# Kernel optimization log

Measured on AMD Instinct MI355X. Metric: run time of the kernel, lower is better.

Reference implementation:

```python
import jax, jax.numpy as jnp
import numpy as np

N, IN_DIM, OUT_DIM, HEADS = 50000, 128, 32, 8
E = 800000
F = OUT_DIM * HEADS  # 256 fused output features
SEM_HID = 128        # SemanticAttention hidden size (HAN default)


def setup_inputs() -> dict:
    key = jax.random.key(0)
    ks = jax.random.split(key, 16)
    inp = {
        "h": jax.random.normal(ks[0], (N, IN_DIM), jnp.float32),
        "src_a": jax.random.randint(ks[1], (E,), 0, N, jnp.int32),
        "dst_a": jax.random.randint(ks[2], (E,), 0, N, jnp.int32),
        "src_b": jax.random.randint(ks[3], (E,), 0, N, jnp.int32),
        "dst_b": jax.random.randint(ks[4], (E,), 0, N, jnp.int32),
    }
    s = 1.0 / np.sqrt(IN_DIM)
    # per-metapath GATConv params
    inp["W_a"] = jax.random.normal(ks[5], (IN_DIM, F), jnp.float32) * s
    inp["al_a"] = jax.random.normal(ks[6], (HEADS, OUT_DIM), jnp.float32) * 0.1
    inp["ar_a"] = jax.random.normal(ks[7], (HEADS, OUT_DIM), jnp.float32) * 0.1
    inp["bias_a"] = jnp.zeros((F,), jnp.float32)
    inp["W_b"] = jax.random.normal(ks[8], (IN_DIM, F), jnp.float32) * s
    inp["al_b"] = jax.random.normal(ks[9], (HEADS, OUT_DIM), jnp.float32) * 0.1
    inp["ar_b"] = jax.random.normal(ks[10], (HEADS, OUT_DIM), jnp.float32) * 0.1
    inp["bias_b"] = jnp.zeros((F,), jnp.float32)
    # semantic attention params
    inp["Wsem"] = jax.random.normal(ks[11], (F, SEM_HID), jnp.float32) / np.sqrt(F)
    inp["bsem"] = jnp.zeros((SEM_HID,), jnp.float32)
    inp["wsem"] = jax.random.normal(ks[12], (SEM_HID,), jnp.float32) / np.sqrt(SEM_HID)
    return inp


def gat_conv(h, src, dst, W, al, ar, bias):
    # h: [N, in_dim] -> feat: [N, H, D]
    feat = (h @ W).reshape(N, HEADS, OUT_DIM)
    el = (feat * al).sum(-1)  # [N, H]
    er = (feat * ar).sum(-1)  # [N, H]
    e = jax.nn.leaky_relu(el[src] + er[dst], 0.2)  # [E, H]
    # edge softmax over incoming edges of each dst node (numerically stable)
    m = jax.ops.segment_max(e, dst, num_segments=N)        # -inf for empty
    ex = jnp.exp(e - m[dst])                               # [E, H]
    denom = jax.ops.segment_sum(ex, dst, num_segments=N)   # [N, H]
    msg = feat[src] * ex[:, :, None]                       # [E, H, D]
    out = jax.ops.segment_sum(msg, dst, num_segments=N)    # [N, H, D]
    out = out / jnp.where(denom > 0, denom, 1.0)[:, :, None]
    return jax.nn.elu(out.reshape(N, F) + bias)


def reference(h, src_a, dst_a, src_b, dst_b,
              W_a, al_a, ar_a, bias_a,
              W_b, al_b, ar_b, bias_b,
              Wsem, bsem, wsem):
    z_a = gat_conv(h, src_a, dst_a, W_a, al_a, ar_a, bias_a)
    z_b = gat_conv(h, src_b, dst_b, W_b, al_b, ar_b, bias_b)
    z = jnp.stack([z_a, z_b], axis=1)                 # [N, M, F]
    q = jnp.tanh(z @ Wsem + bsem) @ wsem              # [N, M]
    beta = jax.nn.softmax(q.mean(axis=0))             # [M]
    return (z * beta[None, :, None]).sum(axis=1)      # [N, F]
```

## Files before the change

kernel.cpp:

```cpp
#include <hip/hip_runtime.h>
#include <stdint.h>

#define NN 50000
#define EE 800000
#define IN_DIM 128
#define OUT_DIM 32
#define HEADS 8
#define FF 256
#define SH 128
#define NPAD 50048
#define FEXT 272
#define NBLK_SCAN 196

typedef short s16x8 __attribute__((ext_vector_type(8)));
typedef float f32x4 __attribute__((ext_vector_type(4)));

__device__ __forceinline__ float b2f(unsigned short u) {
    union { unsigned int i; float f; } v; v.i = ((unsigned int)u) << 16; return v.f;
}
__device__ __forceinline__ unsigned short f2b(float f) {
    union { float f; unsigned int i; } v; v.f = f;
    unsigned int i = v.i;
    unsigned int r = (i + 0x7FFFu + ((i >> 16) & 1u)) >> 16;
    return (unsigned short)r;
}

#define PREP_WSEMT   128
#define PREP_H2B     6256
#define PREP_G       (PREP_WSEMT + PREP_H2B + FEXT + FEXT)

__device__ __forceinline__ void buildBT_one(
    const float* __restrict__ W, const float* __restrict__ al,
    const float* __restrict__ ar, unsigned short* __restrict__ BT,
    int fp, int k)
{
    float v;
    if (fp < FF) {
        v = W[(size_t)k * FF + fp];
    } else if (fp < FF + 8) {
        int hh = fp - FF;
        float s = 0.f;
        #pragma unroll
        for (int d = 0; d < 32; ++d) s += W[(size_t)k * FF + hh * 32 + d] * al[hh * 32 + d];
        v = s;
    } else {
        int hh = fp - FF - 8;
        float s = 0.f;
        #pragma unroll
        for (int d = 0; d < 32; ++d) s += W[(size_t)k * FF + hh * 32 + d] * ar[hh * 32 + d];
        v = s;
    }
    BT[(size_t)fp * IN_DIM + k] = f2b(v);
}

__global__ __launch_bounds__(256) void prep_kernel(
    const float* __restrict__ Wsem, unsigned short* __restrict__ WsemT,
    const float* __restrict__ h, unsigned short* __restrict__ hb,
    const float* __restrict__ W_a, const float* __restrict__ al_a,
    const float* __restrict__ ar_a, unsigned short* __restrict__ BT_a,
    const float* __restrict__ W_b, const float* __restrict__ al_b,
    const float* __restrict__ ar_b, unsigned short* __restrict__ BT_b)
{
    int b = blockIdx.x, t = threadIdx.x;
    if (b < PREP_WSEMT) {
        WsemT[b * FF + t] = f2b(Wsem[(size_t)t * SH + b]);
    } else if (b < PREP_WSEMT + PREP_H2B) {
        int i = ((b - PREP_WSEMT) * 256 + t) * 4;
        int row = i >> 7;
        ushort4 r;
        if (row < NN) {
            float4 v = *(const float4*)(h + i);
            r.x = f2b(v.x); r.y = f2b(v.y); r.z = f2b(v.z); r.w = f2b(v.w);
        } else {
            r.x = r.y = r.z = r.w = 0;
        }
        *(ushort4*)(hb + i) = r;
    } else if (b < PREP_WSEMT + PREP_H2B + FEXT) {
        if (t < IN_DIM) buildBT_one(W_a, al_a, ar_a, BT_a, b - PREP_WSEMT - PREP_H2B, t);
    } else {
        if (t < IN_DIM) buildBT_one(W_b, al_b, ar_b, BT_b, b - PREP_WSEMT - PREP_H2B - FEXT, t);
    }
}

__global__ void rank_both(const int* __restrict__ dst_a, const int* __restrict__ dst_b,
                          int* __restrict__ counts_a, int* __restrict__ counts_b,
                          unsigned short* __restrict__ rank_a, unsigned short* __restrict__ rank_b)
{
    int idx = blockIdx.x * blockDim.x + threadIdx.x;
    if (idx < EE) {
        rank_a[idx] = (unsigned short)atomicAdd(&counts_a[dst_a[idx]], 1);
    } else {
        int e = idx - EE;
        rank_b[e] = (unsigned short)atomicAdd(&counts_b[dst_b[e]], 1);
    }
}

__global__ __launch_bounds__(256) void scan1_both(
    const int* __restrict__ counts_a, const int* __restrict__ counts_b,
    int* __restrict__ offs_a, int* __restrict__ offs_b,
    int* __restrict__ bsums_a, int* __restrict__ bsums_b)
{
    __shared__ int sm[256];
    int bb = blockIdx.x;
    const int* counts = (bb < NBLK_SCAN) ? counts_a : counts_b;
    int* offs  = (bb < NBLK_SCAN) ? offs_a  : offs_b;
    int* bsums = (bb < NBLK_SCAN) ? bsums_a : bsums_b;
    int blk = (bb < NBLK_SCAN) ? bb : bb - NBLK_SCAN;
    int t = threadIdx.x, i = blk * 256 + t;
    int v = (i < NN) ? counts[i] : 0;
    sm[t] = v; __syncthreads();
    for (int d = 1; d < 256; d <<= 1) {
        int x = (t >= d) ? sm[t - d] : 0;
        __syncthreads();
        sm[t] += x;
        __syncthreads();
    }
    if (i < NN) offs[i] = sm[t] - v;
    if (t == 255) bsums[blk] = sm[255];
}

__global__ __launch_bounds__(256) void scan2_both(
    int* __restrict__ bsums_a, int* __restrict__ bsums_b,
    int* __restrict__ offs_a, int* __restrict__ offs_b)
{
    __shared__ int sm[256];
    int* bsums = blockIdx.x ? bsums_b : bsums_a;
    int* offs  = blockIdx.x ? offs_b  : offs_a;
    int t = threadIdx.x;
    int v = (t < NBLK_SCAN) ? bsums[t] : 0;
    sm[t] = v; __syncthreads();
    for (int d = 1; d < 256; d <<= 1) {
        int x = (t >= d) ? sm[t - d] : 0;
        __syncthreads();
        sm[t] += x;
        __syncthreads();
    }
    if (t < NBLK_SCAN) bsums[t] = sm[t] - v;
    if (t == 0) offs[NN] = EE;
}

__global__ __launch_bounds__(256) void scan3_both(
    int* __restrict__ offs_a, int* __restrict__ offs_b,
    const int* __restrict__ bsums_a, const int* __restrict__ bsums_b)
{
    int bb = blockIdx.x;
    int* offs = (bb < NBLK_SCAN) ? offs_a : offs_b;
    const int* bsums = (bb < NBLK_SCAN) ? bsums_a : bsums_b;
    int blk = (bb < NBLK_SCAN) ? bb : bb - NBLK_SCAN;
    int t = threadIdx.x, i = blk * 256 + t;
    if (i < NN) offs[i] += bsums[blk];
}

__global__ void fill_both(const int* __restrict__ src_a, const int* __restrict__ dst_a,
                          const int* __restrict__ src_b, const int* __restrict__ dst_b,
                          const int* __restrict__ offs_a, const int* __restrict__ offs_b,
                          const unsigned short* __restrict__ rank_a,
                          const unsigned short* __restrict__ rank_b,
                          unsigned short* __restrict__ perm_a,
                          unsigned short* __restrict__ perm_b)
{
    int idx = blockIdx.x * blockDim.x + threadIdx.x;
    if (idx < EE) {
        int d = dst_a[idx];
        int slot = offs_a[d] + rank_a[idx];
        perm_a[slot] = (unsigned short)src_a[idx];
    } else {
        int e = idx - EE;
        int d = dst_b[e];
        int slot = offs_b[d] + rank_b[e];
        perm_b[slot] = (unsigned short)src_b[e];
    }
}

__global__ __launch_bounds__(256) void gemm_feat_mfma(
    const unsigned short* __restrict__ hb,
    const unsigned short* __restrict__ BT,
    unsigned short* __restrict__ feat,
    float* __restrict__ el, float* __restrict__ er)
{
    int wave = threadIdx.x >> 6, lane = threadIdx.x & 63;
    int quad = lane >> 4, l16 = lane & 15;
    int nbase = blockIdx.x * 64 + wave * 16;
    int n = nbase + l16;
    const unsigned short* arow = hb + (size_t)n * IN_DIM + quad * 8;
    s16x8 nfr[4];
    #pragma unroll
    for (int kt = 0; kt < 4; ++kt)
        nfr[kt] = *(const s16x8*)(arow + kt * 32);
    bool live = (n < NN);
    #pragma unroll 1
    for (int ft = 0; ft < 17; ++ft) {
        const unsigned short* brow = BT + (size_t)(ft * 16 + l16) * IN_DIM + quad * 8;
        f32x4 c = {0.f, 0.f, 0.f, 0.f};
        #pragma unroll
        for (int kt = 0; kt < 4; ++kt) {
            s16x8 ffr = *(const s16x8*)(brow + kt * 32);
            c = __builtin_amdgcn_mfma_f32_16x16x32_bf16(ffr, nfr[kt], c, 0, 0, 0);
        }
        if (ft < 16) {
            if (live) {
                ushort4 r;
                r.x = f2b(c[0]); r.y = f2b(c[1]); r.z = f2b(c[2]); r.w = f2b(c[3]);
                *(ushort4*)(feat + (size_t)n * FF + ft * 16 + quad * 4) = r;
            }
        } else {
            if (live) {
                #pragma unroll
                for (int r = 0; r < 4; ++r) {
                    int jp = quad * 4 + r;
                    if (jp < 8) el[n * HEADS + jp] = c[r];
                    else        er[n * HEADS + (jp - 8)] = c[r];
                }
            }
        }
    }
}

__global__ __launch_bounds__(256) void pull_kernel(
    const int* __restrict__ offs, const unsigned short* __restrict__ src_perm,
    const float* __restrict__ el, const float* __restrict__ er,
    const unsigned short* __restrict__ feat,
    const float* __restrict__ bias, unsigned short* __restrict__ zb)
{
    int wave = threadIdx.x >> 6;
    int lane = threadIdx.x & 63;
    int n = blockIdx.x * 4 + wave;
    if (n >= NN) return;
    int head = lane >> 3;
    int f0 = lane * 4;
    int j0 = offs[n], j1 = offs[n + 1];
    float ern = er[n * HEADS + head];
    float den = 0.f;
    float a0 = 0.f, a1 = 0.f, a2 = 0.f, a3 = 0.f;

#define EDGE_STEP(S) {                                              \
        float x = el[(S) * HEADS + head] + ern;                     \
        x = fmaxf(x, 0.2f * x);                                     \
        float ex = __expf(x);                                       \
        den += ex;                                                  \
        ushort4 fv = *(const ushort4*)(feat + (size_t)(S) * FF + f0);\
        a0 += b2f(fv.x) * ex;                                       \
        a1 += b2f(fv.y) * ex;                                       \
        a2 += b2f(fv.z) * ex;                                       \
        a3 += b2f(fv.w) * ex; }

    int j = j0;
    for (; j + 8 <= j1; j += 8) {
        int s0 = src_perm[j + 0];
        int s1 = src_perm[j + 1];
        int s2 = src_perm[j + 2];
        int s3 = src_perm[j + 3];
        int s4 = src_perm[j + 4];
        int s5 = src_perm[j + 5];
        int s6 = src_perm[j + 6];
        int s7 = src_perm[j + 7];
        EDGE_STEP(s0); EDGE_STEP(s1); EDGE_STEP(s2); EDGE_STEP(s3);
        EDGE_STEP(s4); EDGE_STEP(s5); EDGE_STEP(s6); EDGE_STEP(s7);
    }
    if (j + 4 <= j1) {
        int s0 = src_perm[j + 0];
        int s1 = src_perm[j + 1];
        int s2 = src_perm[j + 2];
        int s3 = src_perm[j + 3];
        EDGE_STEP(s0); EDGE_STEP(s1); EDGE_STEP(s2); EDGE_STEP(s3);
        j += 4;
    }
    for (; j < j1; ++j) {
        int s = src_perm[j];
        EDGE_STEP(s);
    }
#undef EDGE_STEP

    if (den <= 0.f) den = 1.f;
    float inv = 1.f / den;
    float4 bv = *(const float4*)(bias + f0);
    float o0 = a0 * inv + bv.x;
    float o1 = a1 * inv + bv.y;
    float o2 = a2 * inv + bv.z;
    float o3 = a3 * inv + bv.w;
    ushort4 rb;
    rb.x = f2b((o0 > 0.f) ? o0 : (__expf(o0) - 1.f));
    rb.y = f2b((o1 > 0.f) ? o1 : (__expf(o1) - 1.f));
    rb.z = f2b((o2 > 0.f) ? o2 : (__expf(o2) - 1.f));
    rb.w = f2b((o3 > 0.f) ? o3 : (__expf(o3) - 1.f));
    *(ushort4*)(zb + (size_t)n * FF + f0) = rb;
}

__global__ __launch_bounds__(256) void sem_mfma_kernel(
    const unsigned short* __restrict__ zb,
    const unsigned short* __restrict__ WsemT,
    const float* __restrict__ bsem, const float* __restrict__ wsem,
    float* __restrict__ qsum, int idx)
{
    int wave = threadIdx.x >> 6, lane = threadIdx.x & 63;
    int quad = lane >> 4, l16 = lane & 15;
    int nbase = blockIdx.x * 64 + wave * 16;
    const unsigned short* arow = zb + (size_t)(nbase + l16) * FF + quad * 8;
    s16x8 afr[8];
    #pragma unroll
    for (int kt = 0; kt < 8; ++kt)
        afr[kt] = *(const s16x8*)(arow + kt * 32);
    float qacc = 0.f;
    for (int jt = 0; jt < 8; ++jt) {
        int jj = jt * 16 + l16;
        const unsigned short* brow = WsemT + (size_t)jj * FF + quad * 8;
        f32x4 c = {0.f, 0.f, 0.f, 0.f};
        #pragma unroll
        for (int kt = 0; kt < 8; ++kt) {
            s16x8 bfr = *(const s16x8*)(brow + kt * 32);
            c = __builtin_amdgcn_mfma_f32_16x16x32_bf16(afr[kt], bfr, c, 0, 0, 0);
        }
        float bj = bsem[jj], wj = wsem[jj];
        #pragma unroll
        for (int r = 0; r < 4; ++r) {
            int n = nbase + quad * 4 + r;
            float tv = tanhf(c[r] + bj) * wj;
            qacc += (n < NN) ? tv : 0.f;
        }
    }
    #pragma unroll
    for (int o = 1; o < 64; o <<= 1) qacc += __shfl_xor(qacc, o, 64);
    __shared__ float wsum[4];
    if (lane == 0) wsum[wave] = qacc;
    __syncthreads();
    if (threadIdx.x == 0)
        atomicAdd(&qsum[idx], wsum[0] + wsum[1] + wsum[2] + wsum[3]);
}

__global__ void combine_kernel(const unsigned short* __restrict__ za,
                               const unsigned short* __restrict__ zbm,
                               float* __restrict__ out,
                               const float* __restrict__ qsum)
{
    size_t i = (size_t)blockIdx.x * blockDim.x + threadIdx.x;
    size_t base = i * 4;
    if (base >= (size_t)NN * FF) return;
    float qa = qsum[0] * (1.f / NN), qb = qsum[1] * (1.f / NN);
    float mx = fmaxf(qa, qb);
    float ea = __expf(qa - mx), eb = __expf(qb - mx);
    float inv = 1.f / (ea + eb);
    float b0 = ea * inv, b1 = eb * inv;
    ushort4 va = *(const ushort4*)(za + base);
    ushort4 vb = *(const ushort4*)(zbm + base);
    float4 r;
    r.x = b0 * b2f(va.x) + b1 * b2f(vb.x);
    r.y = b0 * b2f(va.y) + b1 * b2f(vb.y);
    r.z = b0 * b2f(va.z) + b1 * b2f(vb.z);
    r.w = b0 * b2f(va.w) + b1 * b2f(vb.w);
    *(float4*)(out + base) = r;
}

extern "C" void kernel_launch(void* const* d_in, const int* in_sizes, int n_in,
                              void* d_out, int out_size, void* d_ws, size_t ws_size,
                              hipStream_t stream)
{
    const float* h      = (const float*)d_in[0];
    const int* src_a    = (const int*)d_in[1];
    const int* dst_a    = (const int*)d_in[2];
    const int* src_b    = (const int*)d_in[3];
    const int* dst_b    = (const int*)d_in[4];
    const float* W_a    = (const float*)d_in[5];
    const float* al_a   = (const float*)d_in[6];
    const float* ar_a   = (const float*)d_in[7];
    const float* bias_a = (const float*)d_in[8];
    const float* W_b    = (const float*)d_in[9];
    const float* al_b   = (const float*)d_in[10];
    const float* ar_b   = (const float*)d_in[11];
    const float* bias_b = (const float*)d_in[12];
    const float* Wsem   = (const float*)d_in[13];
    const float* bsem   = (const float*)d_in[14];
    const float* wsem   = (const float*)d_in[15];
    float* out = (float*)d_out;

    char* ws = (char*)d_ws;
    size_t o = 0;
    auto alloc = [&](size_t bytes) -> char* {
        char* p = ws + o;
        o += (bytes + 255) & ~(size_t)255;
        return p;
    };
    unsigned short* hb    = (unsigned short*)alloc((size_t)NPAD * IN_DIM * 2);
    unsigned short* BT_a  = (unsigned short*)alloc((size_t)FEXT * IN_DIM * 2);
    unsigned short* BT_b  = (unsigned short*)alloc((size_t)FEXT * IN_DIM * 2);
    unsigned short* feat  = (unsigned short*)alloc((size_t)NN * FF * 2);
    unsigned short* zb_a  = (unsigned short*)alloc((size_t)NPAD * FF * 2);
    unsigned short* zb_b  = (unsigned short*)alloc((size_t)NPAD * FF * 2);
    unsigned short* WsemT = (unsigned short*)alloc((size_t)SH * FF * 2);
    float* el_a    = (float*)alloc((size_t)NN * HEADS * 4);
    float* er_a    = (float*)alloc((size_t)NN * HEADS * 4);
    float* el_b    = (float*)alloc((size_t)NN * HEADS * 4);
    float* er_b    = (float*)alloc((size_t)NN * HEADS * 4);
    int* offs_a    = (int*)alloc((size_t)(NN + 1) * 4);
    int* offs_b    = (int*)alloc((size_t)(NN + 1) * 4);
    int* bsums_a   = (int*)alloc(256 * 4);
    int* bsums_b   = (int*)alloc(256 * 4);
    unsigned short* rank_a = (unsigned short*)alloc((size_t)EE * 2);
    unsigned short* rank_b = (unsigned short*)alloc((size_t)EE * 2);
    unsigned short* perm_a = (unsigned short*)alloc((size_t)EE * 2);
    unsigned short* perm_b = (unsigned short*)alloc((size_t)EE * 2);
    char* zspan0   = ws + o;
    int* counts_a  = (int*)alloc((size_t)NN * 4);
    int* counts_b  = (int*)alloc((size_t)NN * 4);
    float* qsum    = (float*)alloc(8);
    size_t zspan   = (size_t)((ws + o) - zspan0);

    prep_kernel<<<PREP_G, 256, 0, stream>>>(Wsem, WsemT, h, hb,
                                            W_a, al_a, ar_a, BT_a,
                                            W_b, al_b, ar_b, BT_b);
    hipMemsetAsync(zspan0, 0, zspan, stream);
    rank_both<<<2 * (EE / 256), 256, 0, stream>>>(dst_a, dst_b, counts_a, counts_b, rank_a, rank_b);
    scan1_both<<<2 * NBLK_SCAN, 256, 0, stream>>>(counts_a, counts_b, offs_a, offs_b, bsums_a, bsums_b);
    scan2_both<<<2, 256, 0, stream>>>(bsums_a, bsums_b, offs_a, offs_b);
    scan3_both<<<2 * NBLK_SCAN, 256, 0, stream>>>(offs_a, offs_b, bsums_a, bsums_b);
    fill_both<<<2 * (EE / 256), 256, 0, stream>>>(src_a, dst_a, src_b, dst_b,
                                                  offs_a, offs_b, rank_a, rank_b, perm_a, perm_b);
    for (int mp = 0; mp < 2; ++mp) {
        const unsigned short* BT = mp ? BT_b : BT_a;
        const float* bias = mp ? bias_b : bias_a;
        float* el = mp ? el_b : el_a;
        float* er = mp ? er_b : er_a;
        const int* offs = mp ? offs_b : offs_a;
        const unsigned short* perm = mp ? perm_b : perm_a;
        unsigned short* zb = mp ? zb_b : zb_a;

        gemm_feat_mfma<<<NPAD / 64, 256, 0, stream>>>(hb, BT, feat, el, er);
        pull_kernel<<<(NN + 3) / 4, 256, 0, stream>>>(offs, perm, el, er, feat, bias, zb);
        sem_mfma_kernel<<<NPAD / 64, 256, 0, stream>>>(zb, WsemT, bsem, wsem, qsum, mp);
    }
    combine_kernel<<<(int)(((size_t)NN * FF / 4 + 255) / 256), 256, 0, stream>>>(zb_a, zb_b, out, qsum);
}
```

Before: 500.3 us.

## Merge independent stages of both metapaths into shared multi-role kernel launches

Regroups independent work into fewer, larger launches. Edge ranking is co-launched with the weight prep, and the CSR fill with both metapaths' feature GEMMs. The two pull passes and the two semantic-attention passes each become a single launch, which cuts launch count and tail idle between small kernels. The separate h-to-bf16 prepass is removed: the GEMM now reads fp32 h and converts in registers, at the cost of reading h twice and converting it per metapath. It also keeps a second feat buffer so both metapaths can be in flight at once, using more workspace memory.

```diff
diff --git a/kernel.cpp b/kernel.cpp
--- a/kernel.cpp
+++ b/kernel.cpp
@@ -12,6 +12,20 @@
 #define FEXT 272
 #define NBLK_SCAN 196
 
+#define RANK_G   6250
+#define A_WSEMT0 6250
+#define A_BTA0   (A_WSEMT0 + 128)
+#define A_BTB0   (A_BTA0 + FEXT)
+#define A_G      (A_BTB0 + FEXT)
+
+#define B_FILL   6250
+#define GEMM_BLKS 782
+#define B_G      (B_FILL + 2 * GEMM_BLKS)
+
+#define PULL_G   12500
+#define C_G      (2 * PULL_G)
+#define D_G      (2 * GEMM_BLKS)
+
 typedef short s16x8 __attribute__((ext_vector_type(8)));
 typedef float f32x4 __attribute__((ext_vector_type(4)));
 
@@ -24,10 +38,6 @@
     unsigned int r = (i + 0x7FFFu + ((i >> 16) & 1u)) >> 16;
     return (unsigned short)r;
 }
-
-#define PREP_WSEMT   128
-#define PREP_H2B     6256
-#define PREP_G       (PREP_WSEMT + PREP_H2B + FEXT + FEXT)
 
 __device__ __forceinline__ void buildBT_one(
     const float* __restrict__ W, const float* __restrict__ al,
@@ -53,45 +63,32 @@
     BT[(size_t)fp * IN_DIM + k] = f2b(v);
 }
 
-__global__ __launch_bounds__(256) void prep_kernel(
+__global__ __launch_bounds__(256) void megaA(
+    const int* __restrict__ dst_a, const int* __restrict__ dst_b,
+    int* __restrict__ counts_a, int* __restrict__ counts_b,
+    unsigned short* __restrict__ rank_a, unsigned short* __restrict__ rank_b,
     const float* __restrict__ Wsem, unsigned short* __restrict__ WsemT,
-    const float* __restrict__ h, unsigned short* __restrict__ hb,
     const float* __restrict__ W_a, const float* __restrict__ al_a,
     const float* __restrict__ ar_a, unsigned short* __restrict__ BT_a,
     const float* __restrict__ W_b, const float* __restrict__ al_b,
     const float* __restrict__ ar_b, unsigned short* __restrict__ BT_b)
 {
     int b = blockIdx.x, t = threadIdx.x;
-    if (b < PREP_WSEMT) {
-        WsemT[b * FF + t] = f2b(Wsem[(size_t)t * SH + b]);
-    } else if (b < PREP_WSEMT + PREP_H2B) {
-        int i = ((b - PREP_WSEMT) * 256 + t) * 4;
-        int row = i >> 7;
-        ushort4 r;
-        if (row < NN) {
-            float4 v = *(const float4*)(h + i);
-            r.x = f2b(v.x); r.y = f2b(v.y); r.z = f2b(v.z); r.w = f2b(v.w);
+    if (b < RANK_G) {
+        int idx = b * 256 + t;
+        if (idx < EE) {
+            rank_a[idx] = (unsigned short)atomicAdd(&counts_a[dst_a[idx]], 1);
         } else {
-            r.x = r.y = r.z = r.w = 0;
-        }
-        *(ushort4*)(hb + i) = r;
-    } else if (b < PREP_WSEMT + PREP_H2B + FEXT) {
-        if (t < IN_DIM) buildBT_one(W_a, al_a, ar_a, BT_a, b - PREP_WSEMT - PREP_H2B, t);
+            int e = idx - EE;
+            rank_b[e] = (unsigned short)atomicAdd(&counts_b[dst_b[e]], 1);
+        }
+    } else if (b < A_BTA0) {
+        int j = b - A_WSEMT0;
+        WsemT[j * FF + t] = f2b(Wsem[(size_t)t * SH + j]);
+    } else if (b < A_BTB0) {
+        if (t < IN_DIM) buildBT_one(W_a, al_a, ar_a, BT_a, b - A_BTA0, t);
     } else {
-        if (t < IN_DIM) buildBT_one(W_b, al_b, ar_b, BT_b, b - PREP_WSEMT - PREP_H2B - FEXT, t);
-    }
-}
-
-__global__ void rank_both(const int* __restrict__ dst_a, const int* __restrict__ dst_b,
-                          int* __restrict__ counts_a, int* __restrict__ counts_b,
-                          unsigned short* __restrict__ rank_a, unsigned short* __restrict__ rank_b)
-{
-    int idx = blockIdx.x * blockDim.x + threadIdx.x;
-    if (idx < EE) {
-        rank_a[idx] = (unsigned short)atomicAdd(&counts_a[dst_a[idx]], 1);
-    } else {
-        int e = idx - EE;
-        rank_b[e] = (unsigned short)atomicAdd(&counts_b[dst_b[e]], 1);
+        if (t < IN_DIM) buildBT_one(W_b, al_b, ar_b, BT_b, b - A_BTB0, t);
     }
 }
 
@@ -151,42 +148,57 @@
     if (i < NN) offs[i] += bsums[blk];
 }
 
-__global__ void fill_both(const int* __restrict__ src_a, const int* __restrict__ dst_a,
-                          const int* __restrict__ src_b, const int* __restrict__ dst_b,
-                          const int* __restrict__ offs_a, const int* __restrict__ offs_b,
-                          const unsigned short* __restrict__ rank_a,
-                          const unsigned short* __restrict__ rank_b,
-                          unsigned short* __restrict__ perm_a,
-                          unsigned short* __restrict__ perm_b)
-{
-    int idx = blockIdx.x * blockDim.x + threadIdx.x;
-    if (idx < EE) {
-        int d = dst_a[idx];
-        int slot = offs_a[d] + rank_a[idx];
-        perm_a[slot] = (unsigned short)src_a[idx];
-    } else {
-        int e = idx - EE;
-        int d = dst_b[e];
-        int slot = offs_b[d] + rank_b[e];
-        perm_b[slot] = (unsigned short)src_b[e];
-    }
-}
-
-__global__ __launch_bounds__(256) void gemm_feat_mfma(
-    const unsigned short* __restrict__ hb,
-    const unsigned short* __restrict__ BT,
-    unsigned short* __restrict__ feat,
-    float* __restrict__ el, float* __restrict__ er)
-{
-    int wave = threadIdx.x >> 6, lane = threadIdx.x & 63;
+__global__ __launch_bounds__(256) void megaB(
+    const int* __restrict__ src_a, const int* __restrict__ dst_a,
+    const int* __restrict__ src_b, const int* __restrict__ dst_b,
+    const int* __restrict__ offs_a, const int* __restrict__ offs_b,
+    const unsigned short* __restrict__ rank_a, const unsigned short* __restrict__ rank_b,
+    unsigned short* __restrict__ perm_a, unsigned short* __restrict__ perm_b,
+    const float* __restrict__ h,
+    const unsigned short* __restrict__ BT_a, const unsigned short* __restrict__ BT_b,
+    unsigned short* __restrict__ feat_a, unsigned short* __restrict__ feat_b,
+    float* __restrict__ el_a, float* __restrict__ er_a,
+    float* __restrict__ el_b, float* __restrict__ er_b)
+{
+    int b = blockIdx.x, t = threadIdx.x;
+    if (b < B_FILL) {
+        int idx = b * 256 + t;
+        if (idx < EE) {
+            int d = dst_a[idx];
+            perm_a[offs_a[d] + rank_a[idx]] = (unsigned short)src_a[idx];
+        } else {
+            int e = idx - EE;
+            int d = dst_b[e];
+            perm_b[offs_b[d] + rank_b[e]] = (unsigned short)src_b[e];
+        }
+        return;
+    }
+    int g = b - B_FILL;
+    int mp = (g >= GEMM_BLKS);
+    int gb = mp ? g - GEMM_BLKS : g;
+    const unsigned short* BT = mp ? BT_b : BT_a;
+    unsigned short* feat = mp ? feat_b : feat_a;
+    float* el = mp ? el_b : el_a;
+    float* er = mp ? er_b : er_a;
+
+    int wave = t >> 6, lane = t & 63;
     int quad = lane >> 4, l16 = lane & 15;
-    int nbase = blockIdx.x * 64 + wave * 16;
+    int nbase = gb * 64 + wave * 16;
     int n = nbase + l16;
-    const unsigned short* arow = hb + (size_t)n * IN_DIM + quad * 8;
+    int nr = (n < NN) ? n : (NN - 1);
+    const float* hrow = h + (size_t)nr * IN_DIM + quad * 8;
     s16x8 nfr[4];
     #pragma unroll
-    for (int kt = 0; kt < 4; ++kt)
-        nfr[kt] = *(const s16x8*)(arow + kt * 32);
+    for (int kt = 0; kt < 4; ++kt) {
+        float4 p0 = *(const float4*)(hrow + kt * 32);
+        float4 p1 = *(const float4*)(hrow + kt * 32 + 4);
+        s16x8 v;
+        v[0] = (short)f2b(p0.x); v[1] = (short)f2b(p0.y);
+        v[2] = (short)f2b(p0.z); v[3] = (short)f2b(p0.w);
+        v[4] = (short)f2b(p1.x); v[5] = (short)f2b(p1.y);
+        v[6] = (short)f2b(p1.z); v[7] = (short)f2b(p1.w);
+        nfr[kt] = v;
+    }
     bool live = (n < NN);
     #pragma unroll 1
     for (int ft = 0; ft < 17; ++ft) {
@@ -203,28 +215,40 @@
                 r.x = f2b(c[0]); r.y = f2b(c[1]); r.z = f2b(c[2]); r.w = f2b(c[3]);
                 *(ushort4*)(feat + (size_t)n * FF + ft * 16 + quad * 4) = r;
             }
-        } else {
-            if (live) {
-                #pragma unroll
-                for (int r = 0; r < 4; ++r) {
-                    int jp = quad * 4 + r;
-                    if (jp < 8) el[n * HEADS + jp] = c[r];
-                    else        er[n * HEADS + (jp - 8)] = c[r];
-                }
+        } else if (live) {
+            #pragma unroll
+            for (int r = 0; r < 4; ++r) {
+                int jp = quad * 4 + r;
+                if (jp < 8) el[n * HEADS + jp] = c[r];
+                else        er[n * HEADS + (jp - 8)] = c[r];
             }
         }
     }
 }
 
-__global__ __launch_bounds__(256) void pull_kernel(
-    const int* __restrict__ offs, const unsigned short* __restrict__ src_perm,
-    const float* __restrict__ el, const float* __restrict__ er,
-    const unsigned short* __restrict__ feat,
-    const float* __restrict__ bias, unsigned short* __restrict__ zb)
-{
+__global__ __launch_bounds__(256) void megaC(
+    const int* __restrict__ offs_a, const int* __restrict__ offs_b,
+    const unsigned short* __restrict__ perm_a, const unsigned short* __restrict__ perm_b,
+    const float* __restrict__ el_a, const float* __restrict__ er_a,
+    const float* __restrict__ el_b, const float* __restrict__ er_b,
+    const unsigned short* __restrict__ feat_a, const unsigned short* __restrict__ feat_b,
+    const float* __restrict__ bias_a, const float* __restrict__ bias_b,
+    unsigned short* __restrict__ zb_a, unsigned short* __restrict__ zb_b)
+{
+    int bb = blockIdx.x;
+    int mp = (bb >= PULL_G);
+    int blk = mp ? bb - PULL_G : bb;
+    const int* offs = mp ? offs_b : offs_a;
+    const unsigned short* src_perm = mp ? perm_b : perm_a;
+    const float* el = mp ? el_b : el_a;
+    const float* er = mp ? er_b : er_a;
+    const unsigned short* feat = mp ? feat_b : feat_a;
+    const float* bias = mp ? bias_b : bias_a;
+    unsigned short* zb = mp ? zb_b : zb_a;
+
     int wave = threadIdx.x >> 6;
     int lane = threadIdx.x & 63;
-    int n = blockIdx.x * 4 + wave;
+    int n = blk * 4 + wave;
     if (n >= NN) return;
     int head = lane >> 3;
     int f0 = lane * 4;
@@ -286,15 +310,20 @@
     *(ushort4*)(zb + (size_t)n * FF + f0) = rb;
 }
 
-__global__ __launch_bounds__(256) void sem_mfma_kernel(
-    const unsigned short* __restrict__ zb,
+__global__ __launch_bounds__(256) void megaD(
+    const unsigned short* __restrict__ zb_a, const unsigned short* __restrict__ zb_b,
     const unsigned short* __restrict__ WsemT,
     const float* __restrict__ bsem, const float* __restrict__ wsem,
-    float* __restrict__ qsum, int idx)
-{
+    float* __restrict__ qsum)
+{
+    int bb = blockIdx.x;
+    int mp = (bb >= GEMM_BLKS);
+    int blk = mp ? bb - GEMM_BLKS : bb;
+    const unsigned short* zb = mp ? zb_b : zb_a;
+
     int wave = threadIdx.x >> 6, lane = threadIdx.x & 63;
     int quad = lane >> 4, l16 = lane & 15;
-    int nbase = blockIdx.x * 64 + wave * 16;
+    int nbase = blk * 64 + wave * 16;
     const unsigned short* arow = zb + (size_t)(nbase + l16) * FF + quad * 8;
     s16x8 afr[8];
     #pragma unroll
@@ -324,13 +353,13 @@
     if (lane == 0) wsum[wave] = qacc;
     __syncthreads();
     if (threadIdx.x == 0)
-        atomicAdd(&qsum[idx], wsum[0] + wsum[1] + wsum[2] + wsum[3]);
-}
-
-__global__ void combine_kernel(const unsigned short* __restrict__ za,
-                               const unsigned short* __restrict__ zbm,
-                               float* __restrict__ out,
-                               const float* __restrict__ qsum)
+        atomicAdd(&qsum[mp], wsum[0] + wsum[1] + wsum[2] + wsum[3]);
+}
+
+__global__ __launch_bounds__(256) void combine_kernel(
+    const unsigned short* __restrict__ za,
+    const unsigned short* __restrict__ zbm,
+    float* __restrict__ out, const float* __restrict__ qsum)
 {
     size_t i = (size_t)blockIdx.x * blockDim.x + threadIdx.x;
     size_t base = i * 4;
@@ -379,10 +408,10 @@
         o += (bytes + 255) & ~(size_t)255;
         return p;
     };
-    unsigned short* hb    = (unsigned short*)alloc((size_t)NPAD * IN_DIM * 2);
     unsigned short* BT_a  = (unsigned short*)alloc((size_t)FEXT * IN_DIM * 2);
     unsigned short* BT_b  = (unsigned short*)alloc((size_t)FEXT * IN_DIM * 2);
-    unsigned short* feat  = (unsigned short*)alloc((size_t)NN * FF * 2);
+    unsigned short* feat_a = (unsigned short*)alloc((size_t)NN * FF * 2);
+    unsigned short* feat_b = (unsigned short*)alloc((size_t)NN * FF * 2);
     unsigned short* zb_a  = (unsigned short*)alloc((size_t)NPAD * FF * 2);
     unsigned short* zb_b  = (unsigned short*)alloc((size_t)NPAD * FF * 2);
     unsigned short* WsemT = (unsigned short*)alloc((size_t)SH * FF * 2);
@@ -404,28 +433,21 @@
     float* qsum    = (float*)alloc(8);
     size_t zspan   = (size_t)((ws + o) - zspan0);
 
-    prep_kernel<<<PREP_G, 256, 0, stream>>>(Wsem, WsemT, h, hb,
-                                            W_a, al_a, ar_a, BT_a,
-                                            W_b, al_b, ar_b, BT_b);
     hipMemsetAsync(zspan0, 0, zspan, stream);
-    rank_both<<<2 * (EE / 256), 256, 0, stream>>>(dst_a, dst_b, counts_a, counts_b, rank_a, rank_b);
+    megaA<<<A_G, 256, 0, stream>>>(dst_a, dst_b, counts_a, counts_b, rank_a, rank_b,
+                                   Wsem, WsemT,
+                                   W_a, al_a, ar_a, BT_a,
+                                   W_b, al_b, ar_b, BT_b);
     scan1_both<<<2 * NBLK_SCAN, 256, 0, stream>>>(counts_a, counts_b, offs_a, offs_b, bsums_a, bsums_b);
     scan2_both<<<2, 256, 0, stream>>>(bsums_a, bsums_b, offs_a, offs_b);
     scan3_both<<<2 * NBLK_SCAN, 256, 0, stream>>>(offs_a, offs_b, bsums_a, bsums_b);
-    fill_both<<<2 * (EE / 256), 256, 0, stream>>>(src_a, dst_a, src_b, dst_b,
-                                                  offs_a, offs_b, rank_a, rank_b, perm_a, perm_b);
-    for (int mp = 0; mp < 2; ++mp) {
-        const unsigned short* BT = mp ? BT_b : BT_a;
-        const float* bias = mp ? bias_b : bias_a;
-        float* el = mp ? el_b : el_a;
-        float* er = mp ? er_b : er_a;
-        const int* offs = mp ? offs_b : offs_a;
-        const unsigned short* perm = mp ? perm_b : perm_a;
-        unsigned short* zb = mp ? zb_b : zb_a;
-
-        gemm_feat_mfma<<<NPAD / 64, 256, 0, stream>>>(hb, BT, feat, el, er);
-        pull_kernel<<<(NN + 3) / 4, 256, 0, stream>>>(offs, perm, el, er, feat, bias, zb);
-        sem_mfma_kernel<<<NPAD / 64, 256, 0, stream>>>(zb, WsemT, bsem, wsem, qsum, mp);
-    }
+    megaB<<<B_G, 256, 0, stream>>>(src_a, dst_a, src_b, dst_b,
+                                   offs_a, offs_b, rank_a, rank_b, perm_a, perm_b,
+                                   h, BT_a, BT_b, feat_a, feat_b,
+                                   el_a, er_a, el_b, er_b);
+    megaC<<<C_G, 256, 0, stream>>>(offs_a, offs_b, perm_a, perm_b,
+                                   el_a, er_a, el_b, er_b,
+                                   feat_a, feat_b, bias_a, bias_b, zb_a, zb_b);
+    megaD<<<D_G, 256, 0, stream>>>(zb_a, zb_b, WsemT, bsem, wsem, qsum);
     combine_kernel<<<(int)(((size_t)NN * FF / 4 + 255) / 256), 256, 0, stream>>>(zb_a, zb_b, out, qsum);
 }
```

Result: faster. 476.4 us (-4.8%).
